# Kernel tuning notes

Measured on AMD Instinct MI355X. Metric: run time of the kernel, lower is better.

## Reference

```python
import jax, jax.numpy as jnp
import numpy as np

N = 50000       # nodes
E_RAND = 800000 # random edges (avg degree ~16)
K = 64          # edges touching `node`; setup_inputs guarantees exactly K
F = 64          # num_node_features
C = 64          # conv_channels


def setup_inputs() -> dict:
    key = jax.random.key(0)
    ks = jax.random.split(key, 6)
    x = jax.random.normal(ks[0], (N, F), dtype=jnp.float32)
    # random edges avoiding node 0 so exactly the K prepended edges touch node 0
    src = jax.random.randint(ks[1], (E_RAND,), 1, N, dtype=jnp.int64)
    dst = jax.random.randint(ks[2], (E_RAND,), 1, N, dtype=jnp.int64)
    ksrc = jnp.zeros((K,), dtype=jnp.int64)
    kdst = jnp.arange(1, K + 1, dtype=jnp.int64)
    edge_index = jnp.stack([jnp.concatenate([ksrc, src]),
                            jnp.concatenate([kdst, dst])])  # [2, K+E_RAND]
    W1 = jax.random.normal(ks[3], (F, C), jnp.float32) / np.float32(np.sqrt(F))
    b1 = jnp.zeros((C,), jnp.float32)
    W2 = jax.random.normal(ks[4], (C, C), jnp.float32) / np.float32(np.sqrt(C))
    b2 = jnp.zeros((C,), jnp.float32)
    Wr = jax.random.normal(ks[5], (C, 1), jnp.float32) / np.float32(np.sqrt(C))
    br = jnp.zeros((1,), jnp.float32)
    return {"x": x, "edge_index": edge_index, "node": 0,
            "W1": W1, "b1": b1, "W2": W2, "b2": b2, "Wr": Wr, "br": br}


def gcn_conv(x, src, dst, W, b):
    """PyG GCNConv with self-loops already appended to (src, dst).
    out[v] = sum_{(u,v)} deg(u)^-1/2 * deg(v)^-1/2 * (x @ W)[u] + b
    """
    n = x.shape[0]
    xw = x @ W                                              # [N, C]
    deg = jnp.zeros((n,), xw.dtype).at[dst].add(1.0)        # in-degree incl. self-loop
    dinv = jnp.where(deg > 0, jax.lax.rsqrt(deg), 0.0)
    norm = dinv[src] * dinv[dst]                            # [E]
    out = jax.ops.segment_sum(xw[src] * norm[:, None], dst, num_segments=n)
    return out + b


def reference(x, edge_index, node, W1, b1, W2, b2, Wr, br):
    n = x.shape[0]
    loop = jnp.arange(n, dtype=edge_index.dtype)
    src = jnp.concatenate([edge_index[0], loop])  # add self loops (GCNConv default)
    dst = jnp.concatenate([edge_index[1], loop])
    h = jax.nn.relu(gcn_conv(x, src, dst, W1, b1))
    h = jax.nn.relu(gcn_conv(h, src, dst, W2, b2))
    # edges incident to `node` (setup guarantees exactly K such edges)
    s0, d0 = edge_index[0], edge_index[1]
    mask = (s0 == node) | (d0 == node)
    idx = jnp.nonzero(mask, size=K)[0]
    s, d = s0[idx], d0[idx]
    targets = jnp.where(s == node, d, s)  # self-loop (s==d==node) -> node
    score = h[targets] @ Wr + br          # [K, 1]
    score = jax.nn.softmax(score, axis=0)
    return score[:, 0], targets
```

## Files before the change

kernel.cpp:

```cpp
#include <hip/hip_runtime.h>
#include <math.h>

#define KK 64
#define CAP 64
#define NF 4160
#define BMW 1568

__device__ __forceinline__ int fnode_of(int i, const int* tsorted, const int* towner,
                                        const int* tcnt2, const int* tslots) {
    int tp = i / 65, j = i % 65;
    if (j == 0) return tsorted[tp];
    int own = towner[tp];
    int c = tcnt2[own]; if (c > CAP) c = CAP;
    return (j - 1 < c) ? tslots[own * CAP + (j - 1)] : -1;
}

__global__ __launch_bounds__(256) void k_find(const int* __restrict__ ei, int E,
                                              const int* __restrict__ nodep,
                                              int4* __restrict__ zbase, int zcount4,
                                              int* __restrict__ tcount,
                                              int* __restrict__ tpairs) {
    int idx = blockIdx.x * 256 + threadIdx.x;
    if (idx < zcount4) zbase[idx] = make_int4(0, 0, 0, 0);
    int node = nodep[0];
    int n4 = E >> 2;
    if (idx < n4) {
        int4 ss = ((const int4*)ei)[idx];
        int4 dd = ((const int4*)(ei + E))[idx];
        int s[4] = {ss.x, ss.y, ss.z, ss.w};
        int d[4] = {dd.x, dd.y, dd.z, dd.w};
#pragma unroll
        for (int k = 0; k < 4; k++) {
            if (s[k] == node || d[k] == node) {
                int q = atomicAdd(tcount, 1);
                if (q < KK) { int e = idx * 4 + k; tpairs[2 * q] = e; tpairs[2 * q + 1] = (s[k] == node) ? d[k] : s[k]; }
            }
        }
    }
    if (idx == 0) {
        for (int e = n4 * 4; e < E; e++) {
            int s = ei[e], d = ei[E + e];
            if (s == node || d == node) {
                int q = atomicAdd(tcount, 1);
                if (q < KK) { tpairs[2 * q] = e; tpairs[2 * q + 1] = (s == node) ? d : s; }
            }
        }
    }
}

__global__ __launch_bounds__(256) void k_collect_t(const int* __restrict__ ei, int E,
                                                   const int* __restrict__ tpairs,
                                                   int* __restrict__ cnt,
                                                   int* __restrict__ tcnt2,
                                                   int* __restrict__ tslots,
                                                   int* __restrict__ fmapRow,
                                                   int* __restrict__ tsorted_g,
                                                   int* __restrict__ towner_g) {
    __shared__ unsigned int bmask[BMW];
    __shared__ int tnode[KK];
    __shared__ int eidx[KK], tgt[KK], srt[KK];
    int tid = threadIdx.x;
    for (int i = tid; i < BMW; i += 256) bmask[i] = 0u;
    if (tid < KK) { eidx[tid] = tpairs[2 * tid]; tgt[tid] = tpairs[2 * tid + 1]; }
    __syncthreads();
    if (tid < KK) {
        int rank = 0;
        for (int j = 0; j < KK; j++) rank += (eidx[j] < eidx[tid]) ? 1 : 0;
        srt[rank] = tgt[tid];
    }
    __syncthreads();
    if (tid < KK) {
        int mynode = srt[tid];
        int owner = tid;
        for (int j = 0; j < tid; j++) if (srt[j] == mynode) { owner = j; break; }
        tnode[tid] = (owner == tid) ? mynode : -1;
        if (owner == tid) atomicOr(&bmask[mynode >> 5], 1u << (mynode & 31));
        if (blockIdx.x == 0) {
            tsorted_g[tid] = mynode; towner_g[tid] = owner;
            if (owner == tid) atomicCAS(&fmapRow[mynode], 0, tid * 65 + 0 + 1);
        }
    }
    __syncthreads();
    int n4 = E >> 2;
    for (int idx = blockIdx.x * 256 + tid; idx < n4; idx += gridDim.x * 256) {
        int4 ss = ((const int4*)ei)[idx];
        int4 dd = ((const int4*)(ei + E))[idx];
        int s[4] = {ss.x, ss.y, ss.z, ss.w};
        int d[4] = {dd.x, dd.y, dd.z, dd.w};
        atomicAdd(&cnt[d[0]], 1);
        atomicAdd(&cnt[d[1]], 1);
#pragma unroll
        for (int k = 0; k < 4; k++) {
            if ((bmask[d[k] >> 5] >> (d[k] & 31)) & 1u) {
                int f = 0;
                for (int j = 0; j < KK; j++) if (tnode[j] == d[k]) { f = j + 1; break; }
                if (f) {
                    int p = atomicAdd(&tcnt2[f - 1], 1);
                    if (p < CAP) {
                        tslots[(f - 1) * CAP + p] = s[k];
                        atomicCAS(&fmapRow[s[k]], 0, (f - 1) * 65 + (p + 1) + 1);
                    }
                }
            }
        }
    }
    if (blockIdx.x == 0 && tid == 0) {
        for (int e = n4 * 4; e < E; e++) {
            int d = ei[E + e];
            atomicAdd(&cnt[d], 1);
            if ((bmask[d >> 5] >> (d & 31)) & 1u) {
                int f = 0;
                for (int j = 0; j < KK; j++) if (tnode[j] == d) { f = j + 1; break; }
                if (f) {
                    int p = atomicAdd(&tcnt2[f - 1], 1);
                    if (p < CAP) {
                        tslots[(f - 1) * CAP + p] = ei[e];
                        atomicCAS(&fmapRow[ei[e]], 0, (f - 1) * 65 + (p + 1) + 1);
                    }
                }
            }
        }
    }
}

__global__ __launch_bounds__(256) void k_collect_f(const int* __restrict__ ei, int E,
                                                   const int* __restrict__ fmapRow,
                                                   int* __restrict__ cnt,
                                                   int* __restrict__ fcnt,
                                                   int* __restrict__ fslots,
                                                   const int* __restrict__ tsorted,
                                                   const int* __restrict__ towner,
                                                   const int* __restrict__ tcnt2,
                                                   const int* __restrict__ tslots,
                                                   int* __restrict__ ownerCount,
                                                   int2* __restrict__ owners) {
    int idx = blockIdx.x * 256 + threadIdx.x;
    if (idx < NF) {
        int u = fnode_of(idx, tsorted, towner, tcnt2, tslots);
        if (u >= 0 && fmapRow[u] == idx + 1) {
            int p = atomicAdd(ownerCount, 1);
            owners[p] = make_int2(idx, u);
        }
    }
    int n4 = E >> 2;
    if (idx < n4) {
        int4 ss = ((const int4*)ei)[idx];
        int4 dd = ((const int4*)(ei + E))[idx];
        atomicAdd(&cnt[dd.z], 1);
        atomicAdd(&cnt[dd.w], 1);
        int r0 = fmapRow[dd.x], r1 = fmapRow[dd.y], r2 = fmapRow[dd.z], r3 = fmapRow[dd.w];
        if (r0) { int p = atomicAdd(&fcnt[r0 - 1], 1); if (p < CAP) fslots[(size_t)(r0 - 1) * CAP + p] = ss.x; }
        if (r1) { int p = atomicAdd(&fcnt[r1 - 1], 1); if (p < CAP) fslots[(size_t)(r1 - 1) * CAP + p] = ss.y; }
        if (r2) { int p = atomicAdd(&fcnt[r2 - 1], 1); if (p < CAP) fslots[(size_t)(r2 - 1) * CAP + p] = ss.z; }
        if (r3) { int p = atomicAdd(&fcnt[r3 - 1], 1); if (p < CAP) fslots[(size_t)(r3 - 1) * CAP + p] = ss.w; }
    }
    if (idx == 0) {
        for (int e = n4 * 4; e < E; e++) {
            int r = fmapRow[ei[E + e]];
            if (r) { int p = atomicAdd(&fcnt[r - 1], 1); if (p < CAP) fslots[(size_t)(r - 1) * CAP + p] = ei[e]; }
        }
    }
}

__global__ __launch_bounds__(256) void k_layer1(const float* __restrict__ x,
                                                const int2* __restrict__ owners,
                                                const int* __restrict__ ownerCount,
                                                const int* __restrict__ cnt,
                                                const int* __restrict__ fcnt,
                                                const int* __restrict__ fslots,
                                                const float* __restrict__ W1,
                                                const float* __restrict__ b1,
                                                float* __restrict__ h1s) {
    __shared__ __align__(16) float W1s[64 * 64];
    int tid = threadIdx.x;
    int nown = ownerCount[0];
    int ngrp = (nown + 3) >> 2;
    if ((int)blockIdx.x >= ngrp) return;
    for (int j = tid; j < 1024; j += 256) ((float4*)W1s)[j] = ((const float4*)W1)[j];
    __syncthreads();
    int lane = tid & 63;
    for (int g = blockIdx.x; g < ngrp; g += gridDim.x) {
        int idx = g * 4 + (tid >> 6);
        if (idx >= nown) continue;
        int2 ou = owners[idx];
        int i = ou.x, u = ou.y;
        float du = rsqrtf((float)(cnt[u] + 1));
        float acc = du * x[(size_t)u * 64 + lane];
        int c = fcnt[i]; if (c > CAP) c = CAP;
        const int* sl = fslots + (size_t)i * CAP;
        int k = 0;
        for (; k + 4 <= c; k += 4) {
            int u0 = sl[k], u1 = sl[k + 1], u2 = sl[k + 2], u3 = sl[k + 3];
            float f0 = rsqrtf((float)(cnt[u0] + 1));
            float f1 = rsqrtf((float)(cnt[u1] + 1));
            float f2 = rsqrtf((float)(cnt[u2] + 1));
            float f3 = rsqrtf((float)(cnt[u3] + 1));
            acc += f0 * x[(size_t)u0 * 64 + lane] + f1 * x[(size_t)u1 * 64 + lane]
                 + f2 * x[(size_t)u2 * 64 + lane] + f3 * x[(size_t)u3 * 64 + lane];
        }
        for (; k < c; k++) {
            int uu = sl[k];
            acc += rsqrtf((float)(cnt[uu] + 1)) * x[(size_t)uu * 64 + lane];
        }
        float z = du * acc;
        float h = 0.f;
#pragma unroll
        for (int f = 0; f < 64; f++) h += __shfl(z, f) * W1s[f * 64 + lane];
        h = fmaxf(h + b1[lane], 0.f);
        h1s[(size_t)i * 64 + lane] = du * h;
    }
}

__global__ __launch_bounds__(64) void k_score2(const float* __restrict__ h1s,
                                               const int* __restrict__ tsorted,
                                               const int* __restrict__ towner,
                                               const int* __restrict__ tcnt2,
                                               const int* __restrict__ tslots,
                                               const int* __restrict__ fmapRow,
                                               const int* __restrict__ cnt,
                                               const float* __restrict__ W2,
                                               const float* __restrict__ b2,
                                               const float* __restrict__ Wr,
                                               float* __restrict__ sc,
                                               int* __restrict__ done,
                                               float* __restrict__ out) {
    int tp = blockIdx.x;
    int lane = threadIdx.x;
    int t = tsorted[tp];
    float dt = rsqrtf((float)(cnt[t] + 1));
    int own = towner[tp];
    int c = tcnt2[own]; if (c > CAP) c = CAP;
    const int* sl = tslots + own * CAP;
    float z = h1s[(size_t)(fmapRow[t] - 1) * 64 + lane];
#pragma unroll 8
    for (int j = 0; j < c; j++) {
        int u = sl[j];
        int row = fmapRow[u] - 1;
        z += h1s[(size_t)row * 64 + lane];
    }
    z *= dt;
    float acc = 0.f;
#pragma unroll
    for (int f = 0; f < 64; f++) acc += __shfl(z, f) * W2[f * 64 + lane];
    float h2 = fmaxf(acc + b2[lane], 0.f);
    float p = h2 * Wr[lane];
#pragma unroll
    for (int off = 32; off >= 1; off >>= 1) p += __shfl_xor(p, off);
    int last = 0;
    if (lane == 0) {
        __hip_atomic_store(&sc[tp], p, __ATOMIC_RELEASE, __HIP_MEMORY_SCOPE_AGENT);
        last = (__hip_atomic_fetch_add(done, 1, __ATOMIC_ACQ_REL, __HIP_MEMORY_SCOPE_AGENT) == KK - 1) ? 1 : 0;
    }
    last = __shfl(last, 0);
    if (last) {
        float s = __hip_atomic_load(&sc[lane], __ATOMIC_ACQUIRE, __HIP_MEMORY_SCOPE_AGENT);
        float m = s;
#pragma unroll
        for (int off = 32; off >= 1; off >>= 1) m = fmaxf(m, __shfl_xor(m, off));
        float e = __expf(s - m);
        float ssum = e;
#pragma unroll
        for (int off = 32; off >= 1; off >>= 1) ssum += __shfl_xor(ssum, off);
        out[lane] = e / ssum;
        out[KK + lane] = (float)tsorted[lane];
    }
}

extern "C" void kernel_launch(void* const* d_in, const int* in_sizes, int n_in,
                              void* d_out, int out_size, void* d_ws, size_t ws_size,
                              hipStream_t stream) {
    const float* x  = (const float*)d_in[0];
    const int*   ei = (const int*)d_in[1];
    const int*   nodep = (const int*)d_in[2];
    const float* W1 = (const float*)d_in[3];
    const float* b1 = (const float*)d_in[4];
    const float* W2 = (const float*)d_in[5];
    const float* b2 = (const float*)d_in[6];
    const float* Wr = (const float*)d_in[7];
    const float* br = (const float*)d_in[8];
    float* out = (float*)d_out;
    (void)br; (void)n_in; (void)out_size; (void)ws_size;

    int N = in_sizes[0] / 64;
    int E = in_sizes[1] / 2;

    char* w = (char*)d_ws;
    int* cnt     = (int*)w; w += (size_t)N * 4;
    int* fmapRow = (int*)w; w += (size_t)N * 4;
    int* fcnt    = (int*)w; w += (size_t)NF * 4;
    int* tcnt2   = (int*)w; w += KK * 4;
    int* aux     = (int*)w; w += 16;
    int zcount4 = (2 * N + NF + KK + 4) / 4;
    int* tcount = (int*)w; w += 16;
    int* tpairs  = (int*)w; w += 2 * KK * 4;
    int* tsorted = (int*)w; w += KK * 4;
    int* towner  = (int*)w; w += KK * 4;
    int* tslots  = (int*)w; w += (size_t)KK * CAP * 4;
    int2* owners = (int2*)w; w += (size_t)NF * 8;
    int* fslots  = (int*)w; w += (size_t)NF * CAP * 4;
    float* h1s   = (float*)w; w += (size_t)NF * 64 * 4;
    float* sc    = (float*)w; w += KK * 4;

    hipMemsetAsync(tcount, 0, 16, stream);

    int n4 = E >> 2;
    int ebl = (n4 + 255) / 256;
    k_find<<<ebl, 256, 0, stream>>>(ei, E, nodep, (int4*)cnt, zcount4, tcount, tpairs);
    k_collect_t<<<512, 256, 0, stream>>>(ei, E, tpairs, cnt, tcnt2, tslots, fmapRow, tsorted, towner);
    k_collect_f<<<ebl, 256, 0, stream>>>(ei, E, fmapRow, cnt, fcnt, fslots,
                                         tsorted, towner, tcnt2, tslots, &aux[0], owners);
    k_layer1<<<288, 256, 0, stream>>>(x, owners, &aux[0], cnt, fcnt, fslots, W1, b1, h1s);
    k_score2<<<KK, 64, 0, stream>>>(h1s, tsorted, towner, tcnt2, tslots, fmapRow,
                                    cnt, W2, b2, Wr, sc, &aux[1], out);
}
```

Baseline: 145.7 us.

## Fuse layer-1 and scoring into per-target tail kernel; early-exit edge search

Layer-1 aggregation and the layer-2 scoring/softmax kernel are merged into one kernel with one block per target node. Each block recomputes layer-1 features for its target's frontier nodes across four wavefronts, reduces them in shared memory, and then applies W2, Wr and the softmax. This removes the owners list, the h1s global buffer and one kernel launch. The cost is duplicate work for frontier nodes shared between targets, and only 64 blocks in the tail. Separately, k_find skips loading edges once K incident edges have been counted.

```diff
diff --git a/kernel.cpp b/kernel.cpp
--- a/kernel.cpp
+++ b/kernel.cpp
@@ -5,15 +5,6 @@
 #define CAP 64
 #define NF 4160
 #define BMW 1568
-
-__device__ __forceinline__ int fnode_of(int i, const int* tsorted, const int* towner,
-                                        const int* tcnt2, const int* tslots) {
-    int tp = i / 65, j = i % 65;
-    if (j == 0) return tsorted[tp];
-    int own = towner[tp];
-    int c = tcnt2[own]; if (c > CAP) c = CAP;
-    return (j - 1 < c) ? tslots[own * CAP + (j - 1)] : -1;
-}
 
 __global__ __launch_bounds__(256) void k_find(const int* __restrict__ ei, int E,
                                               const int* __restrict__ nodep,
@@ -25,15 +16,18 @@
     int node = nodep[0];
     int n4 = E >> 2;
     if (idx < n4) {
-        int4 ss = ((const int4*)ei)[idx];
-        int4 dd = ((const int4*)(ei + E))[idx];
-        int s[4] = {ss.x, ss.y, ss.z, ss.w};
-        int d[4] = {dd.x, dd.y, dd.z, dd.w};
-#pragma unroll
-        for (int k = 0; k < 4; k++) {
-            if (s[k] == node || d[k] == node) {
-                int q = atomicAdd(tcount, 1);
-                if (q < KK) { int e = idx * 4 + k; tpairs[2 * q] = e; tpairs[2 * q + 1] = (s[k] == node) ? d[k] : s[k]; }
+        int found = __hip_atomic_load(tcount, __ATOMIC_RELAXED, __HIP_MEMORY_SCOPE_AGENT);
+        if (found < KK) {
+            int4 ss = ((const int4*)ei)[idx];
+            int4 dd = ((const int4*)(ei + E))[idx];
+            int s[4] = {ss.x, ss.y, ss.z, ss.w};
+            int d[4] = {dd.x, dd.y, dd.z, dd.w};
+#pragma unroll
+            for (int k = 0; k < 4; k++) {
+                if (s[k] == node || d[k] == node) {
+                    int q = atomicAdd(tcount, 1);
+                    if (q < KK) { int e = idx * 4 + k; tpairs[2 * q] = e; tpairs[2 * q + 1] = (s[k] == node) ? d[k] : s[k]; }
+                }
             }
         }
     }
@@ -127,21 +121,8 @@
                                                    const int* __restrict__ fmapRow,
                                                    int* __restrict__ cnt,
                                                    int* __restrict__ fcnt,
-                                                   int* __restrict__ fslots,
-                                                   const int* __restrict__ tsorted,
-                                                   const int* __restrict__ towner,
-                                                   const int* __restrict__ tcnt2,
-                                                   const int* __restrict__ tslots,
-                                                   int* __restrict__ ownerCount,
-                                                   int2* __restrict__ owners) {
+                                                   int* __restrict__ fslots) {
     int idx = blockIdx.x * 256 + threadIdx.x;
-    if (idx < NF) {
-        int u = fnode_of(idx, tsorted, towner, tcnt2, tslots);
-        if (u >= 0 && fmapRow[u] == idx + 1) {
-            int p = atomicAdd(ownerCount, 1);
-            owners[p] = make_int2(idx, u);
-        }
-    }
     int n4 = E >> 2;
     if (idx < n4) {
         int4 ss = ((const int4*)ei)[idx];
@@ -162,35 +143,52 @@
     }
 }
 
-__global__ __launch_bounds__(256) void k_layer1(const float* __restrict__ x,
-                                                const int2* __restrict__ owners,
-                                                const int* __restrict__ ownerCount,
-                                                const int* __restrict__ cnt,
-                                                const int* __restrict__ fcnt,
-                                                const int* __restrict__ fslots,
-                                                const float* __restrict__ W1,
-                                                const float* __restrict__ b1,
-                                                float* __restrict__ h1s) {
+__global__ __launch_bounds__(256) void k_tail(const float* __restrict__ x,
+                                              const int* __restrict__ tsorted,
+                                              const int* __restrict__ towner,
+                                              const int* __restrict__ tcnt2,
+                                              const int* __restrict__ tslots,
+                                              const int* __restrict__ fmapRow,
+                                              const int* __restrict__ cnt,
+                                              const int* __restrict__ fcnt,
+                                              const int* __restrict__ fslots,
+                                              const float* __restrict__ W1,
+                                              const float* __restrict__ b1,
+                                              const float* __restrict__ W2,
+                                              const float* __restrict__ b2,
+                                              const float* __restrict__ Wr,
+                                              float* __restrict__ sc,
+                                              int* __restrict__ done,
+                                              float* __restrict__ out) {
     __shared__ __align__(16) float W1s[64 * 64];
+    __shared__ __align__(16) float W2s[64 * 64];
+    __shared__ float zred[4][64];
     int tid = threadIdx.x;
-    int nown = ownerCount[0];
-    int ngrp = (nown + 3) >> 2;
-    if ((int)blockIdx.x >= ngrp) return;
-    for (int j = tid; j < 1024; j += 256) ((float4*)W1s)[j] = ((const float4*)W1)[j];
-    __syncthreads();
     int lane = tid & 63;
-    for (int g = blockIdx.x; g < ngrp; g += gridDim.x) {
-        int idx = g * 4 + (tid >> 6);
-        if (idx >= nown) continue;
-        int2 ou = owners[idx];
-        int i = ou.x, u = ou.y;
+    int wv = tid >> 6;
+    for (int j = tid; j < 1024; j += 256) {
+        ((float4*)W1s)[j] = ((const float4*)W1)[j];
+        ((float4*)W2s)[j] = ((const float4*)W2)[j];
+    }
+    int tp = blockIdx.x;
+    int t = tsorted[tp];
+    int own = towner[tp];
+    int c = tcnt2[own]; if (c > CAP) c = CAP;
+    const int* sl = tslots + own * CAP;
+    float b1v = b1[lane];
+    __syncthreads();
+
+    float zt = 0.f;
+    for (int j = wv; j <= c; j += 4) {
+        int u = (j == 0) ? t : sl[j - 1];
+        int ri = fmapRow[u] - 1;
         float du = rsqrtf((float)(cnt[u] + 1));
         float acc = du * x[(size_t)u * 64 + lane];
-        int c = fcnt[i]; if (c > CAP) c = CAP;
-        const int* sl = fslots + (size_t)i * CAP;
+        int cc = fcnt[ri]; if (cc > CAP) cc = CAP;
+        const int* fl = fslots + (size_t)ri * CAP;
         int k = 0;
-        for (; k + 4 <= c; k += 4) {
-            int u0 = sl[k], u1 = sl[k + 1], u2 = sl[k + 2], u3 = sl[k + 3];
+        for (; k + 4 <= cc; k += 4) {
+            int u0 = fl[k], u1 = fl[k + 1], u2 = fl[k + 2], u3 = fl[k + 3];
             float f0 = rsqrtf((float)(cnt[u0] + 1));
             float f1 = rsqrtf((float)(cnt[u1] + 1));
             float f2 = rsqrtf((float)(cnt[u2] + 1));
@@ -198,71 +196,48 @@
             acc += f0 * x[(size_t)u0 * 64 + lane] + f1 * x[(size_t)u1 * 64 + lane]
                  + f2 * x[(size_t)u2 * 64 + lane] + f3 * x[(size_t)u3 * 64 + lane];
         }
-        for (; k < c; k++) {
-            int uu = sl[k];
+        for (; k < cc; k++) {
+            int uu = fl[k];
             acc += rsqrtf((float)(cnt[uu] + 1)) * x[(size_t)uu * 64 + lane];
         }
         float z = du * acc;
         float h = 0.f;
 #pragma unroll
         for (int f = 0; f < 64; f++) h += __shfl(z, f) * W1s[f * 64 + lane];
-        h = fmaxf(h + b1[lane], 0.f);
-        h1s[(size_t)i * 64 + lane] = du * h;
-    }
-}
-
-__global__ __launch_bounds__(64) void k_score2(const float* __restrict__ h1s,
-                                               const int* __restrict__ tsorted,
-                                               const int* __restrict__ towner,
-                                               const int* __restrict__ tcnt2,
-                                               const int* __restrict__ tslots,
-                                               const int* __restrict__ fmapRow,
-                                               const int* __restrict__ cnt,
-                                               const float* __restrict__ W2,
-                                               const float* __restrict__ b2,
-                                               const float* __restrict__ Wr,
-                                               float* __restrict__ sc,
-                                               int* __restrict__ done,
-                                               float* __restrict__ out) {
-    int tp = blockIdx.x;
-    int lane = threadIdx.x;
-    int t = tsorted[tp];
-    float dt = rsqrtf((float)(cnt[t] + 1));
-    int own = towner[tp];
-    int c = tcnt2[own]; if (c > CAP) c = CAP;
-    const int* sl = tslots + own * CAP;
-    float z = h1s[(size_t)(fmapRow[t] - 1) * 64 + lane];
-#pragma unroll 8
-    for (int j = 0; j < c; j++) {
-        int u = sl[j];
-        int row = fmapRow[u] - 1;
-        z += h1s[(size_t)row * 64 + lane];
-    }
-    z *= dt;
-    float acc = 0.f;
-#pragma unroll
-    for (int f = 0; f < 64; f++) acc += __shfl(z, f) * W2[f * 64 + lane];
-    float h2 = fmaxf(acc + b2[lane], 0.f);
-    float p = h2 * Wr[lane];
-#pragma unroll
-    for (int off = 32; off >= 1; off >>= 1) p += __shfl_xor(p, off);
-    int last = 0;
-    if (lane == 0) {
-        __hip_atomic_store(&sc[tp], p, __ATOMIC_RELEASE, __HIP_MEMORY_SCOPE_AGENT);
-        last = (__hip_atomic_fetch_add(done, 1, __ATOMIC_ACQ_REL, __HIP_MEMORY_SCOPE_AGENT) == KK - 1) ? 1 : 0;
-    }
-    last = __shfl(last, 0);
-    if (last) {
-        float s = __hip_atomic_load(&sc[lane], __ATOMIC_ACQUIRE, __HIP_MEMORY_SCOPE_AGENT);
-        float m = s;
-#pragma unroll
-        for (int off = 32; off >= 1; off >>= 1) m = fmaxf(m, __shfl_xor(m, off));
-        float e = __expf(s - m);
-        float ssum = e;
-#pragma unroll
-        for (int off = 32; off >= 1; off >>= 1) ssum += __shfl_xor(ssum, off);
-        out[lane] = e / ssum;
-        out[KK + lane] = (float)tsorted[lane];
+        h = fmaxf(h + b1v, 0.f);
+        zt += du * h;
+    }
+    zred[wv][lane] = zt;
+    __syncthreads();
+
+    if (wv == 0) {
+        float dt = rsqrtf((float)(cnt[t] + 1));
+        float z2 = (zred[0][lane] + zred[1][lane] + zred[2][lane] + zred[3][lane]) * dt;
+        float acc2 = 0.f;
+#pragma unroll
+        for (int f = 0; f < 64; f++) acc2 += __shfl(z2, f) * W2s[f * 64 + lane];
+        float h2 = fmaxf(acc2 + b2[lane], 0.f);
+        float p = h2 * Wr[lane];
+#pragma unroll
+        for (int off = 32; off >= 1; off >>= 1) p += __shfl_xor(p, off);
+        int last = 0;
+        if (lane == 0) {
+            __hip_atomic_store(&sc[tp], p, __ATOMIC_RELEASE, __HIP_MEMORY_SCOPE_AGENT);
+            last = (__hip_atomic_fetch_add(done, 1, __ATOMIC_ACQ_REL, __HIP_MEMORY_SCOPE_AGENT) == KK - 1) ? 1 : 0;
+        }
+        last = __shfl(last, 0);
+        if (last) {
+            float s = __hip_atomic_load(&sc[lane], __ATOMIC_ACQUIRE, __HIP_MEMORY_SCOPE_AGENT);
+            float m = s;
+#pragma unroll
+            for (int off = 32; off >= 1; off >>= 1) m = fmaxf(m, __shfl_xor(m, off));
+            float e = __expf(s - m);
+            float ssum = e;
+#pragma unroll
+            for (int off = 32; off >= 1; off >>= 1) ssum += __shfl_xor(ssum, off);
+            out[lane] = e / ssum;
+            out[KK + lane] = (float)tsorted[lane];
+        }
     }
 }
 
@@ -296,9 +271,7 @@
     int* tsorted = (int*)w; w += KK * 4;
     int* towner  = (int*)w; w += KK * 4;
     int* tslots  = (int*)w; w += (size_t)KK * CAP * 4;
-    int2* owners = (int2*)w; w += (size_t)NF * 8;
     int* fslots  = (int*)w; w += (size_t)NF * CAP * 4;
-    float* h1s   = (float*)w; w += (size_t)NF * 64 * 4;
     float* sc    = (float*)w; w += KK * 4;
 
     hipMemsetAsync(tcount, 0, 16, stream);
@@ -307,9 +280,7 @@
     int ebl = (n4 + 255) / 256;
     k_find<<<ebl, 256, 0, stream>>>(ei, E, nodep, (int4*)cnt, zcount4, tcount, tpairs);
     k_collect_t<<<512, 256, 0, stream>>>(ei, E, tpairs, cnt, tcnt2, tslots, fmapRow, tsorted, towner);
-    k_collect_f<<<ebl, 256, 0, stream>>>(ei, E, fmapRow, cnt, fcnt, fslots,
-                                         tsorted, towner, tcnt2, tslots, &aux[0], owners);
-    k_layer1<<<288, 256, 0, stream>>>(x, owners, &aux[0], cnt, fcnt, fslots, W1, b1, h1s);
-    k_score2<<<KK, 64, 0, stream>>>(h1s, tsorted, towner, tcnt2, tslots, fmapRow,
-                                    cnt, W2, b2, Wr, sc, &aux[1], out);
-}
+    k_collect_f<<<ebl, 256, 0, stream>>>(ei, E, fmapRow, cnt, fcnt, fslots);
+    k_tail<<<KK, 256, 0, stream>>>(x, tsorted, towner, tcnt2, tslots, fmapRow,
+                                   cnt, fcnt, fslots, W1, b1, W2, b2, Wr, sc, &aux[1], out);
+}
```

New measurement: 170.2 us. 1.17x slower.

## Compute degrees only for needed nodes via bitmask in a separate pass

Applied to the files above, without the earlier changes.

Stops counting the in-degree of every node in the collect kernels and instead builds a bitmask of the nodes whose degrees are actually needed (targets, their neighbors, and second-hop sources). A new k_deg pass over the destination array issues atomic increments only for flagged nodes. Source indices are now loaded only when a match is found rather than as a full int4 stream. This removes roughly 800K global atomics but adds a kernel launch and another full read of the dst array.

```diff
diff --git a/kernel.cpp b/kernel.cpp
--- a/kernel.cpp
+++ b/kernel.cpp
@@ -50,10 +50,10 @@
 
 __global__ __launch_bounds__(256) void k_collect_t(const int* __restrict__ ei, int E,
                                                    const int* __restrict__ tpairs,
-                                                   int* __restrict__ cnt,
                                                    int* __restrict__ tcnt2,
                                                    int* __restrict__ tslots,
                                                    int* __restrict__ fmapRow,
+                                                   unsigned int* __restrict__ needed,
                                                    int* __restrict__ tsorted_g,
                                                    int* __restrict__ towner_g) {
     __shared__ unsigned int bmask[BMW];
@@ -77,28 +77,29 @@
         if (owner == tid) atomicOr(&bmask[mynode >> 5], 1u << (mynode & 31));
         if (blockIdx.x == 0) {
             tsorted_g[tid] = mynode; towner_g[tid] = owner;
-            if (owner == tid) atomicCAS(&fmapRow[mynode], 0, tid * 65 + 0 + 1);
+            if (owner == tid) {
+                atomicCAS(&fmapRow[mynode], 0, tid * 65 + 0 + 1);
+                atomicOr(&needed[mynode >> 5], 1u << (mynode & 31));
+            }
         }
     }
     __syncthreads();
     int n4 = E >> 2;
     for (int idx = blockIdx.x * 256 + tid; idx < n4; idx += gridDim.x * 256) {
-        int4 ss = ((const int4*)ei)[idx];
         int4 dd = ((const int4*)(ei + E))[idx];
-        int s[4] = {ss.x, ss.y, ss.z, ss.w};
         int d[4] = {dd.x, dd.y, dd.z, dd.w};
-        atomicAdd(&cnt[d[0]], 1);
-        atomicAdd(&cnt[d[1]], 1);
 #pragma unroll
         for (int k = 0; k < 4; k++) {
             if ((bmask[d[k] >> 5] >> (d[k] & 31)) & 1u) {
                 int f = 0;
                 for (int j = 0; j < KK; j++) if (tnode[j] == d[k]) { f = j + 1; break; }
                 if (f) {
+                    int s = ei[idx * 4 + k];
                     int p = atomicAdd(&tcnt2[f - 1], 1);
                     if (p < CAP) {
-                        tslots[(f - 1) * CAP + p] = s[k];
-                        atomicCAS(&fmapRow[s[k]], 0, (f - 1) * 65 + (p + 1) + 1);
+                        tslots[(f - 1) * CAP + p] = s;
+                        atomicCAS(&fmapRow[s], 0, (f - 1) * 65 + (p + 1) + 1);
+                        atomicOr(&needed[s >> 5], 1u << (s & 31));
                     }
                 }
             }
@@ -107,15 +108,16 @@
     if (blockIdx.x == 0 && tid == 0) {
         for (int e = n4 * 4; e < E; e++) {
             int d = ei[E + e];
-            atomicAdd(&cnt[d], 1);
             if ((bmask[d >> 5] >> (d & 31)) & 1u) {
                 int f = 0;
                 for (int j = 0; j < KK; j++) if (tnode[j] == d) { f = j + 1; break; }
                 if (f) {
+                    int s = ei[e];
                     int p = atomicAdd(&tcnt2[f - 1], 1);
                     if (p < CAP) {
-                        tslots[(f - 1) * CAP + p] = ei[e];
-                        atomicCAS(&fmapRow[ei[e]], 0, (f - 1) * 65 + (p + 1) + 1);
+                        tslots[(f - 1) * CAP + p] = s;
+                        atomicCAS(&fmapRow[s], 0, (f - 1) * 65 + (p + 1) + 1);
+                        atomicOr(&needed[s >> 5], 1u << (s & 31));
                     }
                 }
             }
@@ -125,9 +127,9 @@
 
 __global__ __launch_bounds__(256) void k_collect_f(const int* __restrict__ ei, int E,
                                                    const int* __restrict__ fmapRow,
-                                                   int* __restrict__ cnt,
                                                    int* __restrict__ fcnt,
                                                    int* __restrict__ fslots,
+                                                   unsigned int* __restrict__ needed,
                                                    const int* __restrict__ tsorted,
                                                    const int* __restrict__ towner,
                                                    const int* __restrict__ tcnt2,
@@ -144,20 +146,43 @@
     }
     int n4 = E >> 2;
     if (idx < n4) {
-        int4 ss = ((const int4*)ei)[idx];
         int4 dd = ((const int4*)(ei + E))[idx];
-        atomicAdd(&cnt[dd.z], 1);
-        atomicAdd(&cnt[dd.w], 1);
         int r0 = fmapRow[dd.x], r1 = fmapRow[dd.y], r2 = fmapRow[dd.z], r3 = fmapRow[dd.w];
-        if (r0) { int p = atomicAdd(&fcnt[r0 - 1], 1); if (p < CAP) fslots[(size_t)(r0 - 1) * CAP + p] = ss.x; }
-        if (r1) { int p = atomicAdd(&fcnt[r1 - 1], 1); if (p < CAP) fslots[(size_t)(r1 - 1) * CAP + p] = ss.y; }
-        if (r2) { int p = atomicAdd(&fcnt[r2 - 1], 1); if (p < CAP) fslots[(size_t)(r2 - 1) * CAP + p] = ss.z; }
-        if (r3) { int p = atomicAdd(&fcnt[r3 - 1], 1); if (p < CAP) fslots[(size_t)(r3 - 1) * CAP + p] = ss.w; }
+        if (r0) { int s = ei[idx * 4 + 0]; int p = atomicAdd(&fcnt[r0 - 1], 1);
+                  if (p < CAP) { fslots[(size_t)(r0 - 1) * CAP + p] = s; atomicOr(&needed[s >> 5], 1u << (s & 31)); } }
+        if (r1) { int s = ei[idx * 4 + 1]; int p = atomicAdd(&fcnt[r1 - 1], 1);
+                  if (p < CAP) { fslots[(size_t)(r1 - 1) * CAP + p] = s; atomicOr(&needed[s >> 5], 1u << (s & 31)); } }
+        if (r2) { int s = ei[idx * 4 + 2]; int p = atomicAdd(&fcnt[r2 - 1], 1);
+                  if (p < CAP) { fslots[(size_t)(r2 - 1) * CAP + p] = s; atomicOr(&needed[s >> 5], 1u << (s & 31)); } }
+        if (r3) { int s = ei[idx * 4 + 3]; int p = atomicAdd(&fcnt[r3 - 1], 1);
+                  if (p < CAP) { fslots[(size_t)(r3 - 1) * CAP + p] = s; atomicOr(&needed[s >> 5], 1u << (s & 31)); } }
     }
     if (idx == 0) {
         for (int e = n4 * 4; e < E; e++) {
             int r = fmapRow[ei[E + e]];
-            if (r) { int p = atomicAdd(&fcnt[r - 1], 1); if (p < CAP) fslots[(size_t)(r - 1) * CAP + p] = ei[e]; }
+            if (r) { int s = ei[e]; int p = atomicAdd(&fcnt[r - 1], 1);
+                     if (p < CAP) { fslots[(size_t)(r - 1) * CAP + p] = s; atomicOr(&needed[s >> 5], 1u << (s & 31)); } }
+        }
+    }
+}
+
+__global__ __launch_bounds__(256) void k_deg(const int* __restrict__ ei, int E,
+                                             const unsigned int* __restrict__ needed,
+                                             int* __restrict__ cnt) {
+    int idx = blockIdx.x * 256 + threadIdx.x;
+    int n4 = E >> 2;
+    if (idx < n4) {
+        int4 dd = ((const int4*)(ei + E))[idx];
+        int d[4] = {dd.x, dd.y, dd.z, dd.w};
+#pragma unroll
+        for (int k = 0; k < 4; k++)
+            if ((needed[d[k] >> 5] >> (d[k] & 31)) & 1u)
+                atomicAdd(&cnt[d[k]], 1);
+    }
+    if (idx == 0) {
+        for (int e = n4 * 4; e < E; e++) {
+            int d = ei[E + e];
+            if ((needed[d >> 5] >> (d & 31)) & 1u) atomicAdd(&cnt[d], 1);
         }
     }
 }
@@ -290,7 +315,8 @@
     int* fcnt    = (int*)w; w += (size_t)NF * 4;
     int* tcnt2   = (int*)w; w += KK * 4;
     int* aux     = (int*)w; w += 16;
-    int zcount4 = (2 * N + NF + KK + 4) / 4;
+    unsigned int* needed = (unsigned int*)w; w += BMW * 4;
+    int zcount4 = (2 * N + NF + KK + 4 + BMW) / 4;
     int* tcount = (int*)w; w += 16;
     int* tpairs  = (int*)w; w += 2 * KK * 4;
     int* tsorted = (int*)w; w += KK * 4;
@@ -306,9 +332,10 @@
     int n4 = E >> 2;
     int ebl = (n4 + 255) / 256;
     k_find<<<ebl, 256, 0, stream>>>(ei, E, nodep, (int4*)cnt, zcount4, tcount, tpairs);
-    k_collect_t<<<512, 256, 0, stream>>>(ei, E, tpairs, cnt, tcnt2, tslots, fmapRow, tsorted, towner);
-    k_collect_f<<<ebl, 256, 0, stream>>>(ei, E, fmapRow, cnt, fcnt, fslots,
+    k_collect_t<<<512, 256, 0, stream>>>(ei, E, tpairs, tcnt2, tslots, fmapRow, needed, tsorted, towner);
+    k_collect_f<<<ebl, 256, 0, stream>>>(ei, E, fmapRow, fcnt, fslots, needed,
                                          tsorted, towner, tcnt2, tslots, &aux[0], owners);
+    k_deg<<<ebl, 256, 0, stream>>>(ei, E, needed, cnt);
     k_layer1<<<288, 256, 0, stream>>>(x, owners, &aux[0], cnt, fcnt, fslots, W1, b1, h1s);
     k_score2<<<KK, 64, 0, stream>>>(h1s, tsorted, towner, tcnt2, tslots, fmapRow,
                                     cnt, W2, b2, Wr, sc, &aux[1], out);
```

Result: faster. 142.9 us, median of 2 (-2.0%).

## Merge edge find and target collection into one kernel with grid-wide spin wait

Applied to the files above, without the earlier changes.

Folds the incident-edge search and the first-hop collection into a single persistent kernel of 512 blocks. Blocks publish hits through an atomic counter and spin until all K incident edges are seen, then run the second pass. Each thread keeps its first two edge chunks in registers so it does not reload them. Degree counting moves entirely into this kernel, and the zeroing becomes a memset. This removes one launch and one full edge read, but the spin wait assumes all 512 blocks are resident at once and exactly K incident edges exist, so it can deadlock otherwise.

```diff
diff --git a/kernel.cpp b/kernel.cpp
--- a/kernel.cpp
+++ b/kernel.cpp
@@ -5,6 +5,7 @@
 #define CAP 64
 #define NF 4160
 #define BMW 1568
+#define S1B 512
 
 __device__ __forceinline__ int fnode_of(int i, const int* tsorted, const int* towner,
                                         const int* tcnt2, const int* tslots) {
@@ -15,51 +16,70 @@
     return (j - 1 < c) ? tslots[own * CAP + (j - 1)] : -1;
 }
 
-__global__ __launch_bounds__(256) void k_find(const int* __restrict__ ei, int E,
-                                              const int* __restrict__ nodep,
-                                              int4* __restrict__ zbase, int zcount4,
-                                              int* __restrict__ tcount,
-                                              int* __restrict__ tpairs) {
-    int idx = blockIdx.x * 256 + threadIdx.x;
-    if (idx < zcount4) zbase[idx] = make_int4(0, 0, 0, 0);
-    int node = nodep[0];
-    int n4 = E >> 2;
-    if (idx < n4) {
-        int4 ss = ((const int4*)ei)[idx];
-        int4 dd = ((const int4*)(ei + E))[idx];
-        int s[4] = {ss.x, ss.y, ss.z, ss.w};
-        int d[4] = {dd.x, dd.y, dd.z, dd.w};
-#pragma unroll
-        for (int k = 0; k < 4; k++) {
-            if (s[k] == node || d[k] == node) {
-                int q = atomicAdd(tcount, 1);
-                if (q < KK) { int e = idx * 4 + k; tpairs[2 * q] = e; tpairs[2 * q + 1] = (s[k] == node) ? d[k] : s[k]; }
-            }
-        }
-    }
-    if (idx == 0) {
-        for (int e = n4 * 4; e < E; e++) {
-            int s = ei[e], d = ei[E + e];
-            if (s == node || d == node) {
-                int q = atomicAdd(tcount, 1);
-                if (q < KK) { tpairs[2 * q] = e; tpairs[2 * q + 1] = (s == node) ? d : s; }
-            }
-        }
-    }
-}
-
-__global__ __launch_bounds__(256) void k_collect_t(const int* __restrict__ ei, int E,
-                                                   const int* __restrict__ tpairs,
-                                                   int* __restrict__ cnt,
-                                                   int* __restrict__ tcnt2,
-                                                   int* __restrict__ tslots,
-                                                   int* __restrict__ fmapRow,
-                                                   int* __restrict__ tsorted_g,
-                                                   int* __restrict__ towner_g) {
+__global__ __launch_bounds__(256) void k_scan1(const int* __restrict__ ei, int E,
+                                               const int* __restrict__ nodep,
+                                               int* __restrict__ cnt,
+                                               int* __restrict__ tcnt2,
+                                               int* __restrict__ tslots,
+                                               int* __restrict__ fmapRow,
+                                               int* __restrict__ tcount,
+                                               int* __restrict__ pub,
+                                               int* __restrict__ tpairs,
+                                               int* __restrict__ tsorted_g,
+                                               int* __restrict__ towner_g) {
     __shared__ unsigned int bmask[BMW];
     __shared__ int tnode[KK];
     __shared__ int eidx[KK], tgt[KK], srt[KK];
     int tid = threadIdx.x;
+    int gidx = blockIdx.x * 256 + tid;
+    int gsz = gridDim.x * 256;
+    int node = nodep[0];
+    int n4 = E >> 2;
+
+#define INCIDENT_PUB(sv, dv, ee)                                                          \
+    if ((sv) == node || (dv) == node) {                                                   \
+        int q = atomicAdd(tcount, 1);                                                     \
+        if (q < KK) { tpairs[2 * q] = (ee); tpairs[2 * q + 1] = ((sv) == node) ? (dv) : (sv); } \
+        __hip_atomic_fetch_add(pub, 1, __ATOMIC_RELEASE, __HIP_MEMORY_SCOPE_AGENT);       \
+    }
+
+    int idx0 = gidx, idx1 = gidx + gsz;
+    bool h0 = idx0 < n4, h1 = idx1 < n4;
+    int4 ss0 = make_int4(0,0,0,0), dd0 = ss0, ss1 = ss0, dd1 = ss0;
+    if (h0) { ss0 = ((const int4*)ei)[idx0]; dd0 = ((const int4*)(ei + E))[idx0]; }
+    if (h1) { ss1 = ((const int4*)ei)[idx1]; dd1 = ((const int4*)(ei + E))[idx1]; }
+    if (h0) {
+        atomicAdd(&cnt[dd0.x], 1); atomicAdd(&cnt[dd0.y], 1);
+        atomicAdd(&cnt[dd0.z], 1); atomicAdd(&cnt[dd0.w], 1);
+        INCIDENT_PUB(ss0.x, dd0.x, idx0 * 4 + 0); INCIDENT_PUB(ss0.y, dd0.y, idx0 * 4 + 1);
+        INCIDENT_PUB(ss0.z, dd0.z, idx0 * 4 + 2); INCIDENT_PUB(ss0.w, dd0.w, idx0 * 4 + 3);
+    }
+    if (h1) {
+        atomicAdd(&cnt[dd1.x], 1); atomicAdd(&cnt[dd1.y], 1);
+        atomicAdd(&cnt[dd1.z], 1); atomicAdd(&cnt[dd1.w], 1);
+        INCIDENT_PUB(ss1.x, dd1.x, idx1 * 4 + 0); INCIDENT_PUB(ss1.y, dd1.y, idx1 * 4 + 1);
+        INCIDENT_PUB(ss1.z, dd1.z, idx1 * 4 + 2); INCIDENT_PUB(ss1.w, dd1.w, idx1 * 4 + 3);
+    }
+    for (int idx = gidx + 2 * gsz; idx < n4; idx += gsz) {
+        int4 ss = ((const int4*)ei)[idx];
+        int4 dd = ((const int4*)(ei + E))[idx];
+        atomicAdd(&cnt[dd.x], 1); atomicAdd(&cnt[dd.y], 1);
+        atomicAdd(&cnt[dd.z], 1); atomicAdd(&cnt[dd.w], 1);
+        INCIDENT_PUB(ss.x, dd.x, idx * 4 + 0); INCIDENT_PUB(ss.y, dd.y, idx * 4 + 1);
+        INCIDENT_PUB(ss.z, dd.z, idx * 4 + 2); INCIDENT_PUB(ss.w, dd.w, idx * 4 + 3);
+    }
+    if (gidx == 0) {
+        for (int e = n4 * 4; e < E; e++) {
+            int s = ei[e], d = ei[E + e];
+            atomicAdd(&cnt[d], 1);
+            INCIDENT_PUB(s, d, e);
+        }
+    }
+
+    while (__hip_atomic_load(pub, __ATOMIC_RELAXED, __HIP_MEMORY_SCOPE_AGENT) < KK)
+        __builtin_amdgcn_s_sleep(1);
+    (void)__hip_atomic_load(pub, __ATOMIC_ACQUIRE, __HIP_MEMORY_SCOPE_AGENT);
+
     for (int i = tid; i < BMW; i += 256) bmask[i] = 0u;
     if (tid < KK) { eidx[tid] = tpairs[2 * tid]; tgt[tid] = tpairs[2 * tid + 1]; }
     __syncthreads();
@@ -81,51 +101,42 @@
         }
     }
     __syncthreads();
-    int n4 = E >> 2;
-    for (int idx = blockIdx.x * 256 + tid; idx < n4; idx += gridDim.x * 256) {
+
+#define PHASE2_HIT(dv, sv)                                                                \
+    if ((bmask[(dv) >> 5] >> ((dv) & 31)) & 1u) {                                         \
+        int f = 0;                                                                        \
+        for (int j = 0; j < KK; j++) if (tnode[j] == (dv)) { f = j + 1; break; }          \
+        if (f) {                                                                          \
+            int p = atomicAdd(&tcnt2[f - 1], 1);                                          \
+            if (p < CAP) {                                                                \
+                tslots[(f - 1) * CAP + p] = (sv);                                         \
+                atomicCAS(&fmapRow[(sv)], 0, (f - 1) * 65 + (p + 1) + 1);                 \
+            }                                                                             \
+        }                                                                                 \
+    }
+
+    if (h0) { PHASE2_HIT(dd0.x, ss0.x); PHASE2_HIT(dd0.y, ss0.y);
+              PHASE2_HIT(dd0.z, ss0.z); PHASE2_HIT(dd0.w, ss0.w); }
+    if (h1) { PHASE2_HIT(dd1.x, ss1.x); PHASE2_HIT(dd1.y, ss1.y);
+              PHASE2_HIT(dd1.z, ss1.z); PHASE2_HIT(dd1.w, ss1.w); }
+    for (int idx = gidx + 2 * gsz; idx < n4; idx += gsz) {
         int4 ss = ((const int4*)ei)[idx];
         int4 dd = ((const int4*)(ei + E))[idx];
-        int s[4] = {ss.x, ss.y, ss.z, ss.w};
-        int d[4] = {dd.x, dd.y, dd.z, dd.w};
-        atomicAdd(&cnt[d[0]], 1);
-        atomicAdd(&cnt[d[1]], 1);
-#pragma unroll
-        for (int k = 0; k < 4; k++) {
-            if ((bmask[d[k] >> 5] >> (d[k] & 31)) & 1u) {
-                int f = 0;
-                for (int j = 0; j < KK; j++) if (tnode[j] == d[k]) { f = j + 1; break; }
-                if (f) {
-                    int p = atomicAdd(&tcnt2[f - 1], 1);
-                    if (p < CAP) {
-                        tslots[(f - 1) * CAP + p] = s[k];
-                        atomicCAS(&fmapRow[s[k]], 0, (f - 1) * 65 + (p + 1) + 1);
-                    }
-                }
-            }
-        }
+        PHASE2_HIT(dd.x, ss.x); PHASE2_HIT(dd.y, ss.y);
+        PHASE2_HIT(dd.z, ss.z); PHASE2_HIT(dd.w, ss.w);
     }
     if (blockIdx.x == 0 && tid == 0) {
         for (int e = n4 * 4; e < E; e++) {
-            int d = ei[E + e];
-            atomicAdd(&cnt[d], 1);
-            if ((bmask[d >> 5] >> (d & 31)) & 1u) {
-                int f = 0;
-                for (int j = 0; j < KK; j++) if (tnode[j] == d) { f = j + 1; break; }
-                if (f) {
-                    int p = atomicAdd(&tcnt2[f - 1], 1);
-                    if (p < CAP) {
-                        tslots[(f - 1) * CAP + p] = ei[e];
-                        atomicCAS(&fmapRow[ei[e]], 0, (f - 1) * 65 + (p + 1) + 1);
-                    }
-                }
-            }
-        }
-    }
+            int d = ei[E + e], s = ei[e];
+            PHASE2_HIT(d, s);
+        }
+    }
+#undef INCIDENT_PUB
+#undef PHASE2_HIT
 }
 
 __global__ __launch_bounds__(256) void k_collect_f(const int* __restrict__ ei, int E,
                                                    const int* __restrict__ fmapRow,
-                                                   int* __restrict__ cnt,
                                                    int* __restrict__ fcnt,
                                                    int* __restrict__ fslots,
                                                    const int* __restrict__ tsorted,
@@ -144,20 +155,22 @@
     }
     int n4 = E >> 2;
     if (idx < n4) {
-        int4 ss = ((const int4*)ei)[idx];
         int4 dd = ((const int4*)(ei + E))[idx];
-        atomicAdd(&cnt[dd.z], 1);
-        atomicAdd(&cnt[dd.w], 1);
         int r0 = fmapRow[dd.x], r1 = fmapRow[dd.y], r2 = fmapRow[dd.z], r3 = fmapRow[dd.w];
-        if (r0) { int p = atomicAdd(&fcnt[r0 - 1], 1); if (p < CAP) fslots[(size_t)(r0 - 1) * CAP + p] = ss.x; }
-        if (r1) { int p = atomicAdd(&fcnt[r1 - 1], 1); if (p < CAP) fslots[(size_t)(r1 - 1) * CAP + p] = ss.y; }
-        if (r2) { int p = atomicAdd(&fcnt[r2 - 1], 1); if (p < CAP) fslots[(size_t)(r2 - 1) * CAP + p] = ss.z; }
-        if (r3) { int p = atomicAdd(&fcnt[r3 - 1], 1); if (p < CAP) fslots[(size_t)(r3 - 1) * CAP + p] = ss.w; }
+        if (r0) { int s = ei[idx * 4 + 0]; int p = atomicAdd(&fcnt[r0 - 1], 1);
+                  if (p < CAP) fslots[(size_t)(r0 - 1) * CAP + p] = s; }
+        if (r1) { int s = ei[idx * 4 + 1]; int p = atomicAdd(&fcnt[r1 - 1], 1);
+                  if (p < CAP) fslots[(size_t)(r1 - 1) * CAP + p] = s; }
+        if (r2) { int s = ei[idx * 4 + 2]; int p = atomicAdd(&fcnt[r2 - 1], 1);
+                  if (p < CAP) fslots[(size_t)(r2 - 1) * CAP + p] = s; }
+        if (r3) { int s = ei[idx * 4 + 3]; int p = atomicAdd(&fcnt[r3 - 1], 1);
+                  if (p < CAP) fslots[(size_t)(r3 - 1) * CAP + p] = s; }
     }
     if (idx == 0) {
         for (int e = n4 * 4; e < E; e++) {
             int r = fmapRow[ei[E + e]];
-            if (r) { int p = atomicAdd(&fcnt[r - 1], 1); if (p < CAP) fslots[(size_t)(r - 1) * CAP + p] = ei[e]; }
+            if (r) { int s = ei[e]; int p = atomicAdd(&fcnt[r - 1], 1);
+                     if (p < CAP) fslots[(size_t)(r - 1) * CAP + p] = s; }
         }
     }
 }
@@ -290,8 +303,7 @@
     int* fcnt    = (int*)w; w += (size_t)NF * 4;
     int* tcnt2   = (int*)w; w += KK * 4;
     int* aux     = (int*)w; w += 16;
-    int zcount4 = (2 * N + NF + KK + 4) / 4;
-    int* tcount = (int*)w; w += 16;
+    size_t zbytes = (size_t)(2 * N + NF + KK) * 4 + 16;
     int* tpairs  = (int*)w; w += 2 * KK * 4;
     int* tsorted = (int*)w; w += KK * 4;
     int* towner  = (int*)w; w += KK * 4;
@@ -301,13 +313,13 @@
     float* h1s   = (float*)w; w += (size_t)NF * 64 * 4;
     float* sc    = (float*)w; w += KK * 4;
 
-    hipMemsetAsync(tcount, 0, 16, stream);
+    hipMemsetAsync(cnt, 0, zbytes, stream);
 
     int n4 = E >> 2;
     int ebl = (n4 + 255) / 256;
-    k_find<<<ebl, 256, 0, stream>>>(ei, E, nodep, (int4*)cnt, zcount4, tcount, tpairs);
-    k_collect_t<<<512, 256, 0, stream>>>(ei, E, tpairs, cnt, tcnt2, tslots, fmapRow, tsorted, towner);
-    k_collect_f<<<ebl, 256, 0, stream>>>(ei, E, fmapRow, cnt, fcnt, fslots,
+    k_scan1<<<S1B, 256, 0, stream>>>(ei, E, nodep, cnt, tcnt2, tslots, fmapRow,
+                                     &aux[2], &aux[3], tpairs, tsorted, towner);
+    k_collect_f<<<ebl, 256, 0, stream>>>(ei, E, fmapRow, fcnt, fslots,
                                          tsorted, towner, tcnt2, tslots, &aux[0], owners);
     k_layer1<<<288, 256, 0, stream>>>(x, owners, &aux[0], cnt, fcnt, fslots, W1, b1, h1s);
     k_score2<<<KK, 64, 0, stream>>>(h1s, tsorted, towner, tcnt2, tslots, fmapRow,
```

Result: slower. 175.3 us (+20.3%).
